# Kernel optimization log

Measured on AMD Instinct MI355X. Metric: run time of the kernel, lower is better.

The kernel has to match this reference:

```python
import jax, jax.numpy as jnp
import numpy as np

NUM_HEADS = 32
NUM_KV_HEADS = 8
HEAD_DIM = 128
SCALE = 1.0 / np.sqrt(HEAD_DIM)
BATCH = 16
MAX_CTX = 2048
NUM_SLOTS = BATCH * MAX_CTX + BATCH  # 32784; last BATCH slots are the write targets


def setup_inputs() -> dict:
    key = jax.random.key(0)
    ks = jax.random.split(key, 8)
    q = jax.random.normal(ks[0], (BATCH, NUM_HEADS, HEAD_DIM), dtype=jnp.float32)
    k = jax.random.normal(ks[1], (BATCH, NUM_KV_HEADS, HEAD_DIM), dtype=jnp.float32)
    v = jax.random.normal(ks[2], (BATCH, NUM_KV_HEADS, HEAD_DIM), dtype=jnp.float32)
    k_cache = jax.random.normal(ks[3], (NUM_SLOTS, NUM_KV_HEADS, HEAD_DIM), dtype=jnp.float32)
    v_cache = jax.random.normal(ks[4], (NUM_SLOTS, NUM_KV_HEADS, HEAD_DIM), dtype=jnp.float32)
    # each decode token writes its new kv into a fresh slot at the end of the pool
    slot_mapping = (BATCH * MAX_CTX + jnp.arange(BATCH)).astype(jnp.int64)
    # sparse-controller-selected active slots per request (paged, irregular)
    active_slots = jax.random.randint(ks[5], (BATCH, MAX_CTX), 0, NUM_SLOTS).astype(jnp.int64)
    # make the current token's slot the last active slot of its own request
    active_slots = active_slots.at[:, -1].set(slot_mapping)
    context_lens = jax.random.randint(ks[6], (BATCH,), 1, MAX_CTX + 1).astype(jnp.int64)
    return {
        "q": q, "k": k, "v": v,
        "k_cache": k_cache, "v_cache": v_cache,
        "slot_mapping": slot_mapping,
        "active_slots": active_slots,
        "context_lens": context_lens,
    }


def _attend(q, k, v, k_cache, v_cache, slot_mapping, active_slots, context_lens):
    # store_kvcache: scatter new k/v into flat slot cache; slot == -1 is skipped
    safe_slots = jnp.where(slot_mapping < 0, NUM_SLOTS, slot_mapping)  # OOB -> dropped
    kc = k_cache.at[safe_slots].set(k, mode="drop")
    vc = v_cache.at[safe_slots].set(v, mode="drop")

    # paged gather of the per-request active KV pages
    K = kc[active_slots]  # [B, L, Hkv, D]
    V = vc[active_slots]  # [B, L, Hkv, D]

    B, H, D = q.shape
    G = H // NUM_KV_HEADS  # GQA group size
    qg = q.reshape(B, NUM_KV_HEADS, G, D)

    # flash-decode stage1+stage2 == numerically-stable softmax attention over active slots
    scores = jnp.einsum("bkgd,blkd->bkgl", qg, K) * SCALE  # [B, Hkv, G, L]
    valid = jnp.arange(active_slots.shape[1])[None, :] < context_lens[:, None]  # [B, L]
    scores = jnp.where(valid[:, None, None, :], scores, jnp.float32(-1e30))
    p = jax.nn.softmax(scores, axis=-1)
    o = jnp.einsum("bkgl,blkd->bkgd", p, V).reshape(B, H, D)
    return o


def reference(q, k, v, k_cache, v_cache, slot_mapping, active_slots, context_lens):
    return _attend(q, k, v, k_cache, v_cache, slot_mapping, active_slots, context_lens)
```

## Files before the change

kernel.cpp:

```cpp
#include <hip/hip_runtime.h>
#include <hip/hip_bf16.h>
#include <float.h>

#define B 16
#define H 32
#define HKV 8
#define G 4
#define D 128
#define LMAX 2048
#define SCALE 0.08838834764831844f
#define THR 8.0f

template <int CHUNK>
__global__ __launch_bounds__(64) void attn_partial(
    const float* __restrict__ q,
    const float* __restrict__ kin,
    const float* __restrict__ vin,
    const float* __restrict__ kc,
    const float* __restrict__ vc,
    const int*  __restrict__ slot_mapping,
    const int*  __restrict__ active_slots,
    const int*  __restrict__ context_lens,
    float* __restrict__ part_o,
    float* __restrict__ part_ml)
{
    constexpr int NSPLIT = LMAX / CHUNK;
    const int tid   = threadIdx.x;
    const int split = blockIdx.x % NSPLIT;
    const int h     = (blockIdx.x / NSPLIT) % HKV;
    const int b     = blockIdx.x / (NSPLIT * HKV);

    const int ctx   = context_lens[b];
    const int start = split * CHUNK;
    int nvalid = ctx - start;
    if (nvalid > CHUNK) nvalid = CHUNK;

    const size_t pbase = ((size_t)(b * HKV + h) * NSPLIT + split) * G;

    if (nvalid <= 0) {
        if (tid < G * 2) part_ml[pbase * 2 + tid] = (tid & 1) ? 0.f : -FLT_MAX;
        return;
    }

    __shared__ const float* kp[CHUNK];
    __shared__ const float* vp[CHUNK];
    __shared__ float  red[8][G][D];
    __shared__ float2 mlred[8][G];

    int smv[16];
#pragma unroll
    for (int j = 0; j < 16; ++j) smv[j] = slot_mapping[j];
    for (int li = tid; li < nvalid; li += 64) {
        const int s = active_slots[b * LMAX + start + li];
        int ov = -1;
#pragma unroll
        for (int j = 0; j < 16; ++j)
            if (smv[j] == s) ov = j;
        kp[li] = (ov >= 0) ? kin + ((size_t)ov * HKV + h) * D : kc + ((size_t)s * HKV + h) * D;
        vp[li] = (ov >= 0) ? vin + ((size_t)ov * HKV + h) * D : vc + ((size_t)s * HKV + h) * D;
    }

    const int grp   = tid >> 3;
    const int lane8 = tid & 7;

    float4 qv[G][4];
#pragma unroll
    for (int g = 0; g < G; ++g) {
        const float* qp = q + ((size_t)(b * H + h * G + g)) * D;
#pragma unroll
        for (int j = 0; j < 4; ++j) {
            float4 t = *(const float4*)(qp + j * 32 + lane8 * 4);
            qv[g][j] = make_float4(t.x * SCALE, t.y * SCALE, t.z * SCALE, t.w * SCALE);
        }
    }

    float m0 = -1e30f, m1 = -1e30f, m2 = -1e30f, m3 = -1e30f;
    float l0 = 0.f, l1 = 0.f, l2 = 0.f, l3 = 0.f;
    float4 o0[4] = {}, o1[4] = {}, o2[4] = {}, o3[4] = {};

    constexpr int ITERS = CHUNK / 8;
#pragma unroll 2
    for (int it = 0; it < ITERS; ++it) {
        const int r  = it * 8 + grp;
        const int rl = (r < nvalid) ? r : nvalid - 1;
        const float* kb = kp[rl];
        const float* vb = vp[rl];
        float4 kv[4], vv[4];
#pragma unroll
        for (int j = 0; j < 4; ++j) kv[j] = *(const float4*)(kb + j * 32 + lane8 * 4);
#pragma unroll
        for (int j = 0; j < 4; ++j) vv[j] = *(const float4*)(vb + j * 32 + lane8 * 4);

        float pd0 = 0.f, pd1 = 0.f, pd2 = 0.f, pd3 = 0.f;
#pragma unroll
        for (int j = 0; j < 4; ++j) {
            pd0 += kv[j].x * qv[0][j].x + kv[j].y * qv[0][j].y + kv[j].z * qv[0][j].z + kv[j].w * qv[0][j].w;
            pd1 += kv[j].x * qv[1][j].x + kv[j].y * qv[1][j].y + kv[j].z * qv[1][j].z + kv[j].w * qv[1][j].w;
            pd2 += kv[j].x * qv[2][j].x + kv[j].y * qv[2][j].y + kv[j].z * qv[2][j].z + kv[j].w * qv[2][j].w;
            pd3 += kv[j].x * qv[3][j].x + kv[j].y * qv[3][j].y + kv[j].z * qv[3][j].z + kv[j].w * qv[3][j].w;
        }
#pragma unroll
        for (int msk = 1; msk < 8; msk <<= 1) {
            pd0 += __shfl_xor(pd0, msk, 8);
            pd1 += __shfl_xor(pd1, msk, 8);
            pd2 += __shfl_xor(pd2, msk, 8);
            pd3 += __shfl_xor(pd3, msk, 8);
        }

        const bool valid = (r < nvalid);
        const float s0 = valid ? pd0 : -1e30f;
        const float s1 = valid ? pd1 : -1e30f;
        const float s2 = valid ? pd2 : -1e30f;
        const float s3 = valid ? pd3 : -1e30f;

        if (s0 > m0 + THR) {
            const float sc = __expf(m0 - s0); l0 *= sc; m0 = s0;
#pragma unroll
            for (int j = 0; j < 4; ++j) { o0[j].x *= sc; o0[j].y *= sc; o0[j].z *= sc; o0[j].w *= sc; }
        }
        if (s1 > m1 + THR) {
            const float sc = __expf(m1 - s1); l1 *= sc; m1 = s1;
#pragma unroll
            for (int j = 0; j < 4; ++j) { o1[j].x *= sc; o1[j].y *= sc; o1[j].z *= sc; o1[j].w *= sc; }
        }
        if (s2 > m2 + THR) {
            const float sc = __expf(m2 - s2); l2 *= sc; m2 = s2;
#pragma unroll
            for (int j = 0; j < 4; ++j) { o2[j].x *= sc; o2[j].y *= sc; o2[j].z *= sc; o2[j].w *= sc; }
        }
        if (s3 > m3 + THR) {
            const float sc = __expf(m3 - s3); l3 *= sc; m3 = s3;
#pragma unroll
            for (int j = 0; j < 4; ++j) { o3[j].x *= sc; o3[j].y *= sc; o3[j].z *= sc; o3[j].w *= sc; }
        }

        const float p0 = __expf(s0 - m0);
        const float p1 = __expf(s1 - m1);
        const float p2 = __expf(s2 - m2);
        const float p3 = __expf(s3 - m3);
        l0 += p0; l1 += p1; l2 += p2; l3 += p3;
#pragma unroll
        for (int j = 0; j < 4; ++j) {
            o0[j].x += p0 * vv[j].x; o0[j].y += p0 * vv[j].y; o0[j].z += p0 * vv[j].z; o0[j].w += p0 * vv[j].w;
            o1[j].x += p1 * vv[j].x; o1[j].y += p1 * vv[j].y; o1[j].z += p1 * vv[j].z; o1[j].w += p1 * vv[j].w;
            o2[j].x += p2 * vv[j].x; o2[j].y += p2 * vv[j].y; o2[j].z += p2 * vv[j].z; o2[j].w += p2 * vv[j].w;
            o3[j].x += p3 * vv[j].x; o3[j].y += p3 * vv[j].y; o3[j].z += p3 * vv[j].z; o3[j].w += p3 * vv[j].w;
        }
    }

#pragma unroll
    for (int j = 0; j < 4; ++j) {
        *(float4*)&red[grp][0][j * 32 + lane8 * 4] = o0[j];
        *(float4*)&red[grp][1][j * 32 + lane8 * 4] = o1[j];
        *(float4*)&red[grp][2][j * 32 + lane8 * 4] = o2[j];
        *(float4*)&red[grp][3][j * 32 + lane8 * 4] = o3[j];
    }
    if (lane8 == 0) {
        mlred[grp][0] = make_float2(m0, l0);
        mlred[grp][1] = make_float2(m1, l1);
        mlred[grp][2] = make_float2(m2, l2);
        mlred[grp][3] = make_float2(m3, l3);
    }
    __syncthreads();

#pragma unroll
    for (int g = 0; g < G; ++g) {
        float Mg = -1e30f;
#pragma unroll
        for (int gr = 0; gr < 8; ++gr) Mg = fmaxf(Mg, mlred[gr][g].x);
        float Lg = 0.f, acc0 = 0.f, acc1 = 0.f;
#pragma unroll
        for (int gr = 0; gr < 8; ++gr) {
            const float2 ml = mlred[gr][g];
            const float w = __expf(ml.x - Mg);
            Lg += ml.y * w;
            acc0 += red[gr][g][tid]      * w;
            acc1 += red[gr][g][tid + 64] * w;
        }
        part_o[(pbase + g) * D + tid]      = acc0;
        part_o[(pbase + g) * D + tid + 64] = acc1;
        if (tid == 0) {
            part_ml[(pbase + g) * 2 + 0] = Mg;
            part_ml[(pbase + g) * 2 + 1] = Lg;
        }
    }
}

__global__ __launch_bounds__(256) void attn_reduce(
    const float* __restrict__ part_o,
    const float* __restrict__ part_ml,
    float* __restrict__ out,
    int nsplit)
{
    const int g = blockIdx.x & 3;
    const int h = (blockIdx.x >> 2) & 7;
    const int b = blockIdx.x >> 5;
    const int d  = threadIdx.x & 127;
    const int sp = threadIdx.x >> 7;

    __shared__ float mlds[64], llds[64];
    __shared__ float red[128];
    __shared__ float lred;
    const size_t base = (size_t)(b * HKV + h) * nsplit;

    for (int s = threadIdx.x; s < nsplit; s += 256) {
        mlds[s] = part_ml[((base + s) * G + g) * 2 + 0];
        llds[s] = part_ml[((base + s) * G + g) * 2 + 1];
    }
    __syncthreads();

    float M = -FLT_MAX;
    for (int s = 0; s < nsplit; ++s)
        if (llds[s] > 0.f) M = fmaxf(M, mlds[s]);

    float L = 0.f, acc = 0.f;
    for (int s = sp; s < nsplit; s += 2) {
        const float l = llds[s];
        if (l > 0.f) {
            const float e = __expf(mlds[s] - M);
            L += l * e;
            acc += e * part_o[((base + s) * G + g) * D + d];
        }
    }
    if (sp == 1) {
        red[d] = acc;
        if (d == 0) lred = L;
    }
    __syncthreads();
    if (sp == 0) {
        acc += red[d];
        L   += lred;
        out[((size_t)(b * H) + h * G + g) * D + d] = acc / (L > 0.f ? L : 1.f);
    }
}

extern "C" void kernel_launch(void* const* d_in, const int* in_sizes, int n_in,
                              void* d_out, int out_size, void* d_ws, size_t ws_size,
                              hipStream_t stream) {
    const float* q  = (const float*)d_in[0];
    const float* k  = (const float*)d_in[1];
    const float* v  = (const float*)d_in[2];
    const float* kc = (const float*)d_in[3];
    const float* vc = (const float*)d_in[4];
    const int* slot_mapping = (const int*)d_in[5];
    const int* active_slots = (const int*)d_in[6];
    const int* context_lens = (const int*)d_in[7];
    float* out = (float*)d_out;

    const size_t perSplit = (size_t)B * HKV * (G * D + G * 2) * sizeof(float);
    int nsplit = 8;
    if (ws_size >= 32 * perSplit)      nsplit = 32;
    else if (ws_size >= 16 * perSplit) nsplit = 16;

    float* part_o  = (float*)d_ws;
    float* part_ml = part_o + (size_t)B * HKV * nsplit * G * D;

    if (nsplit == 32) {
        attn_partial<64><<<B * HKV * 32, 64, 0, stream>>>(
            q, k, v, kc, vc, slot_mapping, active_slots, context_lens, part_o, part_ml);
    } else if (nsplit == 16) {
        attn_partial<128><<<B * HKV * 16, 64, 0, stream>>>(
            q, k, v, kc, vc, slot_mapping, active_slots, context_lens, part_o, part_ml);
    } else {
        attn_partial<256><<<B * HKV * 8, 64, 0, stream>>>(
            q, k, v, kc, vc, slot_mapping, active_slots, context_lens, part_o, part_ml);
    }
    attn_reduce<<<B * HKV * G, 256, 0, stream>>>(part_o, part_ml, out, nsplit);
}
```

Measured before the change: 42.09 us.

## Restructure partial attention to 32-lane rows with prefetch and finer splits

The partial kernel now has each half-wave of 32 lanes own a full 128-wide K/V row, so the wave handles two rows per iteration instead of eight. The next row's K/V loads are software-pipelined one iteration ahead, the shared-memory cross-group reduction is replaced by a single xor-32 shuffle merge, and the loop runs only over valid rows. It also adds a 64-split configuration with chunk 32 and sets launch bounds to 4 blocks per CU. The aim is to cut register pressure, LDS traffic and wasted work on padded rows while raising parallelism, at the cost of less memory-level parallelism per wave and a larger reduce stage.

```diff
diff --git a/kernel.cpp b/kernel.cpp
--- a/kernel.cpp
+++ b/kernel.cpp
@@ -12,7 +12,7 @@
 #define THR 8.0f
 
 template <int CHUNK>
-__global__ __launch_bounds__(64) void attn_partial(
+__global__ __launch_bounds__(64, 4) void attn_partial(
     const float* __restrict__ q,
     const float* __restrict__ kin,
     const float* __restrict__ vin,
@@ -44,69 +44,61 @@
 
     __shared__ const float* kp[CHUNK];
     __shared__ const float* vp[CHUNK];
-    __shared__ float  red[8][G][D];
-    __shared__ float2 mlred[8][G];
-
-    int smv[16];
-#pragma unroll
-    for (int j = 0; j < 16; ++j) smv[j] = slot_mapping[j];
+
     for (int li = tid; li < nvalid; li += 64) {
         const int s = active_slots[b * LMAX + start + li];
         int ov = -1;
 #pragma unroll
         for (int j = 0; j < 16; ++j)
-            if (smv[j] == s) ov = j;
+            if (slot_mapping[j] == s) ov = j;
         kp[li] = (ov >= 0) ? kin + ((size_t)ov * HKV + h) * D : kc + ((size_t)s * HKV + h) * D;
         vp[li] = (ov >= 0) ? vin + ((size_t)ov * HKV + h) * D : vc + ((size_t)s * HKV + h) * D;
     }
-
-    const int grp   = tid >> 3;
-    const int lane8 = tid & 7;
-
-    float4 qv[G][4];
+    __syncthreads();
+
+    const int grp2 = tid >> 5;
+    const int ln   = tid & 31;
+    const int nv1  = nvalid - 1;
+
+    float4 qv[G];
 #pragma unroll
     for (int g = 0; g < G; ++g) {
-        const float* qp = q + ((size_t)(b * H + h * G + g)) * D;
-#pragma unroll
-        for (int j = 0; j < 4; ++j) {
-            float4 t = *(const float4*)(qp + j * 32 + lane8 * 4);
-            qv[g][j] = make_float4(t.x * SCALE, t.y * SCALE, t.z * SCALE, t.w * SCALE);
-        }
+        float4 t = *(const float4*)(q + ((size_t)(b * H + h * G + g)) * D + ln * 4);
+        qv[g] = make_float4(t.x * SCALE, t.y * SCALE, t.z * SCALE, t.w * SCALE);
     }
 
     float m0 = -1e30f, m1 = -1e30f, m2 = -1e30f, m3 = -1e30f;
     float l0 = 0.f, l1 = 0.f, l2 = 0.f, l3 = 0.f;
-    float4 o0[4] = {}, o1[4] = {}, o2[4] = {}, o3[4] = {};
-
-    constexpr int ITERS = CHUNK / 8;
-#pragma unroll 2
-    for (int it = 0; it < ITERS; ++it) {
-        const int r  = it * 8 + grp;
-        const int rl = (r < nvalid) ? r : nvalid - 1;
-        const float* kb = kp[rl];
-        const float* vb = vp[rl];
-        float4 kv[4], vv[4];
+    float4 o0 = {0,0,0,0}, o1 = {0,0,0,0}, o2 = {0,0,0,0}, o3 = {0,0,0,0};
+
+    const int iters = (nvalid + 1) >> 1;
+
+    int ra = grp2;     ra = (ra <= nv1) ? ra : nv1;
+    int rb = 2 + grp2; rb = (rb <= nv1) ? rb : nv1;
+    const float* kB = kp[rb];
+    const float* vB = vp[rb];
+    float4 ka = *(const float4*)(kp[ra] + ln * 4);
+    float4 va = *(const float4*)(vp[ra] + ln * 4);
+
+    for (int it = 0; it < iters; ++it) {
+        float4 kb = *(const float4*)(kB + ln * 4);
+        float4 vb = *(const float4*)(vB + ln * 4);
+        int rn = (it + 2) * 2 + grp2; rn = (rn <= nv1) ? rn : nv1;
+        const float* kN = kp[rn];
+        const float* vN = vp[rn];
+
+        const int r = it * 2 + grp2;
+        float pd0 = ka.x * qv[0].x + ka.y * qv[0].y + ka.z * qv[0].z + ka.w * qv[0].w;
+        float pd1 = ka.x * qv[1].x + ka.y * qv[1].y + ka.z * qv[1].z + ka.w * qv[1].w;
+        float pd2 = ka.x * qv[2].x + ka.y * qv[2].y + ka.z * qv[2].z + ka.w * qv[2].w;
+        float pd3 = ka.x * qv[3].x + ka.y * qv[3].y + ka.z * qv[3].z + ka.w * qv[3].w;
 #pragma unroll
-        for (int j = 0; j < 4; ++j) kv[j] = *(const float4*)(kb + j * 32 + lane8 * 4);
-#pragma unroll
-        for (int j = 0; j < 4; ++j) vv[j] = *(const float4*)(vb + j * 32 + lane8 * 4);
-
-        float pd0 = 0.f, pd1 = 0.f, pd2 = 0.f, pd3 = 0.f;
-#pragma unroll
-        for (int j = 0; j < 4; ++j) {
-            pd0 += kv[j].x * qv[0][j].x + kv[j].y * qv[0][j].y + kv[j].z * qv[0][j].z + kv[j].w * qv[0][j].w;
-            pd1 += kv[j].x * qv[1][j].x + kv[j].y * qv[1][j].y + kv[j].z * qv[1][j].z + kv[j].w * qv[1][j].w;
-            pd2 += kv[j].x * qv[2][j].x + kv[j].y * qv[2][j].y + kv[j].z * qv[2][j].z + kv[j].w * qv[2][j].w;
-            pd3 += kv[j].x * qv[3][j].x + kv[j].y * qv[3][j].y + kv[j].z * qv[3][j].z + kv[j].w * qv[3][j].w;
-        }
-#pragma unroll
-        for (int msk = 1; msk < 8; msk <<= 1) {
-            pd0 += __shfl_xor(pd0, msk, 8);
-            pd1 += __shfl_xor(pd1, msk, 8);
-            pd2 += __shfl_xor(pd2, msk, 8);
-            pd3 += __shfl_xor(pd3, msk, 8);
-        }
-
+        for (int msk = 1; msk < 32; msk <<= 1) {
+            pd0 += __shfl_xor(pd0, msk);
+            pd1 += __shfl_xor(pd1, msk);
+            pd2 += __shfl_xor(pd2, msk);
+            pd3 += __shfl_xor(pd3, msk);
+        }
         const bool valid = (r < nvalid);
         const float s0 = valid ? pd0 : -1e30f;
         const float s1 = valid ? pd1 : -1e30f;
@@ -115,23 +107,19 @@
 
         if (s0 > m0 + THR) {
             const float sc = __expf(m0 - s0); l0 *= sc; m0 = s0;
-#pragma unroll
-            for (int j = 0; j < 4; ++j) { o0[j].x *= sc; o0[j].y *= sc; o0[j].z *= sc; o0[j].w *= sc; }
+            o0.x *= sc; o0.y *= sc; o0.z *= sc; o0.w *= sc;
         }
         if (s1 > m1 + THR) {
             const float sc = __expf(m1 - s1); l1 *= sc; m1 = s1;
-#pragma unroll
-            for (int j = 0; j < 4; ++j) { o1[j].x *= sc; o1[j].y *= sc; o1[j].z *= sc; o1[j].w *= sc; }
+            o1.x *= sc; o1.y *= sc; o1.z *= sc; o1.w *= sc;
         }
         if (s2 > m2 + THR) {
             const float sc = __expf(m2 - s2); l2 *= sc; m2 = s2;
-#pragma unroll
-            for (int j = 0; j < 4; ++j) { o2[j].x *= sc; o2[j].y *= sc; o2[j].z *= sc; o2[j].w *= sc; }
+            o2.x *= sc; o2.y *= sc; o2.z *= sc; o2.w *= sc;
         }
         if (s3 > m3 + THR) {
             const float sc = __expf(m3 - s3); l3 *= sc; m3 = s3;
-#pragma unroll
-            for (int j = 0; j < 4; ++j) { o3[j].x *= sc; o3[j].y *= sc; o3[j].z *= sc; o3[j].w *= sc; }
+            o3.x *= sc; o3.y *= sc; o3.z *= sc; o3.w *= sc;
         }
 
         const float p0 = __expf(s0 - m0);
@@ -139,50 +127,51 @@
         const float p2 = __expf(s2 - m2);
         const float p3 = __expf(s3 - m3);
         l0 += p0; l1 += p1; l2 += p2; l3 += p3;
-#pragma unroll
-        for (int j = 0; j < 4; ++j) {
-            o0[j].x += p0 * vv[j].x; o0[j].y += p0 * vv[j].y; o0[j].z += p0 * vv[j].z; o0[j].w += p0 * vv[j].w;
-            o1[j].x += p1 * vv[j].x; o1[j].y += p1 * vv[j].y; o1[j].z += p1 * vv[j].z; o1[j].w += p1 * vv[j].w;
-            o2[j].x += p2 * vv[j].x; o2[j].y += p2 * vv[j].y; o2[j].z += p2 * vv[j].z; o2[j].w += p2 * vv[j].w;
-            o3[j].x += p3 * vv[j].x; o3[j].y += p3 * vv[j].y; o3[j].z += p3 * vv[j].z; o3[j].w += p3 * vv[j].w;
-        }
-    }
-
-#pragma unroll
-    for (int j = 0; j < 4; ++j) {
-        *(float4*)&red[grp][0][j * 32 + lane8 * 4] = o0[j];
-        *(float4*)&red[grp][1][j * 32 + lane8 * 4] = o1[j];
-        *(float4*)&red[grp][2][j * 32 + lane8 * 4] = o2[j];
-        *(float4*)&red[grp][3][j * 32 + lane8 * 4] = o3[j];
-    }
-    if (lane8 == 0) {
-        mlred[grp][0] = make_float2(m0, l0);
-        mlred[grp][1] = make_float2(m1, l1);
-        mlred[grp][2] = make_float2(m2, l2);
-        mlred[grp][3] = make_float2(m3, l3);
-    }
-    __syncthreads();
-
-#pragma unroll
-    for (int g = 0; g < G; ++g) {
-        float Mg = -1e30f;
-#pragma unroll
-        for (int gr = 0; gr < 8; ++gr) Mg = fmaxf(Mg, mlred[gr][g].x);
-        float Lg = 0.f, acc0 = 0.f, acc1 = 0.f;
-#pragma unroll
-        for (int gr = 0; gr < 8; ++gr) {
-            const float2 ml = mlred[gr][g];
-            const float w = __expf(ml.x - Mg);
-            Lg += ml.y * w;
-            acc0 += red[gr][g][tid]      * w;
-            acc1 += red[gr][g][tid + 64] * w;
-        }
-        part_o[(pbase + g) * D + tid]      = acc0;
-        part_o[(pbase + g) * D + tid + 64] = acc1;
-        if (tid == 0) {
-            part_ml[(pbase + g) * 2 + 0] = Mg;
-            part_ml[(pbase + g) * 2 + 1] = Lg;
-        }
+        o0.x += p0 * va.x; o0.y += p0 * va.y; o0.z += p0 * va.z; o0.w += p0 * va.w;
+        o1.x += p1 * va.x; o1.y += p1 * va.y; o1.z += p1 * va.z; o1.w += p1 * va.w;
+        o2.x += p2 * va.x; o2.y += p2 * va.y; o2.z += p2 * va.z; o2.w += p2 * va.w;
+        o3.x += p3 * va.x; o3.y += p3 * va.y; o3.z += p3 * va.z; o3.w += p3 * va.w;
+
+        ka = kb; va = vb; kB = kN; vB = vN;
+    }
+
+    {
+        const float M0 = fmaxf(m0, __shfl_xor(m0, 32));
+        const float M1 = fmaxf(m1, __shfl_xor(m1, 32));
+        const float M2 = fmaxf(m2, __shfl_xor(m2, 32));
+        const float M3 = fmaxf(m3, __shfl_xor(m3, 32));
+        const float w0 = __expf(m0 - M0);
+        const float w1 = __expf(m1 - M1);
+        const float w2 = __expf(m2 - M2);
+        const float w3 = __expf(m3 - M3);
+        l0 *= w0; l1 *= w1; l2 *= w2; l3 *= w3;
+        l0 += __shfl_xor(l0, 32); l1 += __shfl_xor(l1, 32);
+        l2 += __shfl_xor(l2, 32); l3 += __shfl_xor(l3, 32);
+        o0.x *= w0; o0.y *= w0; o0.z *= w0; o0.w *= w0;
+        o1.x *= w1; o1.y *= w1; o1.z *= w1; o1.w *= w1;
+        o2.x *= w2; o2.y *= w2; o2.z *= w2; o2.w *= w2;
+        o3.x *= w3; o3.y *= w3; o3.z *= w3; o3.w *= w3;
+        o0.x += __shfl_xor(o0.x, 32); o0.y += __shfl_xor(o0.y, 32);
+        o0.z += __shfl_xor(o0.z, 32); o0.w += __shfl_xor(o0.w, 32);
+        o1.x += __shfl_xor(o1.x, 32); o1.y += __shfl_xor(o1.y, 32);
+        o1.z += __shfl_xor(o1.z, 32); o1.w += __shfl_xor(o1.w, 32);
+        o2.x += __shfl_xor(o2.x, 32); o2.y += __shfl_xor(o2.y, 32);
+        o2.z += __shfl_xor(o2.z, 32); o2.w += __shfl_xor(o2.w, 32);
+        o3.x += __shfl_xor(o3.x, 32); o3.y += __shfl_xor(o3.y, 32);
+        o3.z += __shfl_xor(o3.z, 32); o3.w += __shfl_xor(o3.w, 32);
+        m0 = M0; m1 = M1; m2 = M2; m3 = M3;
+    }
+
+    if (grp2 == 0) {
+        *(float4*)(part_o + (pbase + 0) * D + ln * 4) = o0;
+        *(float4*)(part_o + (pbase + 1) * D + ln * 4) = o1;
+    } else {
+        *(float4*)(part_o + (pbase + 2) * D + ln * 4) = o2;
+        *(float4*)(part_o + (pbase + 3) * D + ln * 4) = o3;
+    }
+    if (tid == 0) {
+        *(float4*)&part_ml[pbase * 2 + 0] = make_float4(m0, l0, m1, l1);
+        *(float4*)&part_ml[pbase * 2 + 4] = make_float4(m2, l2, m3, l3);
     }
 }
 
@@ -249,13 +238,17 @@
 
     const size_t perSplit = (size_t)B * HKV * (G * D + G * 2) * sizeof(float);
     int nsplit = 8;
-    if (ws_size >= 32 * perSplit)      nsplit = 32;
+    if (ws_size >= 64 * perSplit)      nsplit = 64;
+    else if (ws_size >= 32 * perSplit) nsplit = 32;
     else if (ws_size >= 16 * perSplit) nsplit = 16;
 
     float* part_o  = (float*)d_ws;
     float* part_ml = part_o + (size_t)B * HKV * nsplit * G * D;
 
-    if (nsplit == 32) {
+    if (nsplit == 64) {
+        attn_partial<32><<<B * HKV * 64, 64, 0, stream>>>(
+            q, k, v, kc, vc, slot_mapping, active_slots, context_lens, part_o, part_ml);
+    } else if (nsplit == 32) {
         attn_partial<64><<<B * HKV * 32, 64, 0, stream>>>(
             q, k, v, kc, vc, slot_mapping, active_slots, context_lens, part_o, part_ml);
     } else if (nsplit == 16) {
```

New measurement: 51.17 us. +21.6%, slower.
